# Kernel tuning notes

Measured on AMD Instinct MI355X. Metric: run time of the kernel, lower is better.

## Reference

```python
import jax, jax.numpy as jnp
import numpy as np


def _prelu(x, a):
    return jnp.where(x >= 0, x, a * x)


def _conv1x1(x, w, b, a):
    # x: [N,C,H,W], w: [O,C], b: [O] -> PReLU(conv1x1(x))
    y = jnp.einsum('oc,nchw->nohw', w, x) + b[None, :, None, None]
    return _prelu(y, a)


def setup_inputs() -> dict:
    key = jax.random.key(0)
    ks = jax.random.split(key, 8)
    N, C, H, W = 4, 128, 64, 64
    Cr = C // 2  # reduction=2
    sC = 1.0 / np.sqrt(C)
    x = jax.random.normal(ks[0], (N, C, H, W), dtype=jnp.float32)
    w1 = jax.random.normal(ks[1], (Cr, C), dtype=jnp.float32) * sC
    b1 = jnp.zeros((Cr,), dtype=jnp.float32)
    a1 = jnp.asarray(0.25, dtype=jnp.float32)  # PReLU (single shared slope)
    w2 = jax.random.normal(ks[2], (Cr, C), dtype=jnp.float32) * sC
    b2 = jnp.zeros((Cr,), dtype=jnp.float32)
    a2 = jnp.asarray(0.25, dtype=jnp.float32)
    wa = jax.random.normal(ks[3], (C, C), dtype=jnp.float32) * sC
    ba = jnp.zeros((C,), dtype=jnp.float32)
    aa = jnp.asarray(0.25, dtype=jnp.float32)
    return {"x": x, "w1": w1, "b1": b1, "a1": a1,
            "w2": w2, "b2": b2, "a2": a2,
            "wa": wa, "ba": ba, "aa": aa}


def reference(x, w1, b1, a1, w2, b2, a2, wa, ba, aa):
    N, C, H, W = x.shape
    HW = H * W
    e1 = _conv1x1(x, w1, b1, a1).reshape(N, -1, HW)   # [N,Cr,HW]
    e2 = _conv1x1(x, w2, b2, a2).reshape(N, -1, HW)   # [N,Cr,HW]
    asm = _conv1x1(x, wa, ba, aa).reshape(N, C, HW)   # [N,C,HW]
    # ksize=1: per-channel outer products summed over channels == single contraction
    score = jnp.einsum('nci,ncj->nij', e1, e2)        # [N,HW,HW]
    score = jax.nn.softmax(score, axis=2)
    out = jnp.einsum('nij,ncj->nci', score, asm)      # [N,C,HW]
    return out.reshape(N, C, H, W)
```

## Files before the change

### kernel.cpp

```cpp
#include <hip/hip_runtime.h>
#include <hip/hip_bf16.h>
#include <stdint.h>


typedef float   f32x16 __attribute__((ext_vector_type(16)));
typedef __bf16  bf16x8 __attribute__((ext_vector_type(8)));
typedef __bf16  bf16x2 __attribute__((ext_vector_type(2)));
typedef unsigned int u32x4 __attribute__((ext_vector_type(4)));
typedef unsigned int u32x2 __attribute__((ext_vector_type(2)));

#define L2E 1.4426950408889634f

#define Q_OFF   (0u)
#define KF_OFF  (2u << 20)
#define VF_OFF  (4u << 20)
#define DEN_OFF (8u << 20)
#define WH_OFF  ((8u << 20) + (1u << 19))
#define WL_OFF  (WH_OFF + (1u << 16))
#define OP_OFF  (9u << 20)

__device__ inline unsigned short f2bf(float f) {
  unsigned u = __builtin_bit_cast(unsigned, f);
  return (unsigned short)((u + 0x7FFFu + ((u >> 16) & 1u)) >> 16);
}
__device__ inline float bf2f(unsigned short h) {
  unsigned u = ((unsigned)h) << 16;
  return __builtin_bit_cast(float, u);
}

__global__ void wcast_kernel(const float* __restrict__ w1, const float* __restrict__ w2,
                             const float* __restrict__ wa, char* __restrict__ ws) {
  int idx = blockIdx.x * 256 + threadIdx.x;
  unsigned short* WH = (unsigned short*)(ws + WH_OFF);
  unsigned short* WL = (unsigned short*)(ws + WL_OFF);
#pragma unroll
  for (int r = 0; r < 4; ++r) {
    int i = r * 8192 + idx;
    int oc = i >> 7, c = i & 127;
    float v = oc < 64 ? w1[oc * 128 + c]
            : (oc < 128 ? w2[(oc - 64) * 128 + c] : wa[(oc - 128) * 128 + c]);
    unsigned short h = f2bf(v);
    WH[i] = h;
    WL[i] = f2bf(v - bf2f(h));
  }
}

__global__ __launch_bounds__(256) void conv_kernel(
    const float* __restrict__ x, char* __restrict__ ws,
    const float* __restrict__ b1, const float* __restrict__ a1,
    const float* __restrict__ b2, const float* __restrict__ a2,
    const float* __restrict__ ba, const float* __restrict__ aa) {
  int bid = blockIdx.x;
  int n = bid >> 7, st = bid & 127;
  int sb = st * 32;
  int tid = threadIdx.x;
  int wid = tid >> 6, lane = tid & 63, l31 = lane & 31, hi = lane >> 5;

  __shared__ float xl[128][36];
  __shared__ float tl[2][64][33];
  float* vl = (float*)xl;

  const float* xb = x + (size_t)n * 128 * 4096;
#pragma unroll
  for (int it = 0; it < 4; ++it) {
    int flat4 = tid + 256 * it;
    int c = flat4 >> 3, s4 = flat4 & 7;
    float4 v = *(const float4*)(xb + (size_t)c * 4096 + sb + s4 * 4);
    *(float4*)&xl[c][s4 * 4] = v;
  }
  __syncthreads();

  const char* WH = ws + WH_OFF;
  const char* WL = ws + WL_OFF;
  int oc0 = wid * 64;

  f32x16 acc[2];
  acc[0] = 0.f; acc[1] = 0.f;
#pragma unroll
  for (int c0 = 0; c0 < 8; ++c0) {
    __bf16 eh[8], el[8];
#pragma unroll
    for (int j = 0; j < 8; ++j) {
      float v = xl[c0 * 16 + hi * 8 + j][l31];
      __bf16 h = (__bf16)v;
      eh[j] = h;
      el[j] = (__bf16)(v - (float)h);
    }
    bf16x8 xh = {eh[0], eh[1], eh[2], eh[3], eh[4], eh[5], eh[6], eh[7]};
    bf16x8 xlo = {el[0], el[1], el[2], el[3], el[4], el[5], el[6], el[7]};
#pragma unroll
    for (int mb = 0; mb < 2; ++mb) {
      size_t wo = (size_t)(oc0 + mb * 32 + l31) * 256 + c0 * 32 + hi * 16;
      bf16x8 wh = *(const bf16x8*)(WH + wo);
      bf16x8 wl = *(const bf16x8*)(WL + wo);
      acc[mb] = __builtin_amdgcn_mfma_f32_32x32x16_bf16(wh, xh, acc[mb], 0, 0, 0);
      acc[mb] = __builtin_amdgcn_mfma_f32_32x32x16_bf16(wh, xlo, acc[mb], 0, 0, 0);
      acc[mb] = __builtin_amdgcn_mfma_f32_32x32x16_bf16(wl, xh, acc[mb], 0, 0, 0);
    }
  }
  __syncthreads();

  if (wid < 2) {
    const float* bb = wid ? b2 : b1;
    float slope = wid ? a2[0] : a1[0];
    float scl = wid ? 1.0f : L2E;
#pragma unroll
    for (int mb = 0; mb < 2; ++mb)
#pragma unroll
      for (int reg = 0; reg < 16; ++reg) {
        int row = mb * 32 + (reg & 3) + 8 * (reg >> 2) + 4 * hi;
        float y = acc[mb][reg] + bb[row];
        y = fmaxf(y, 0.f) + slope * fminf(y, 0.f);
        tl[wid][row][l31] = y * scl;
      }
  } else {
    float slope = aa[0];
#pragma unroll
    for (int mb = 0; mb < 2; ++mb)
#pragma unroll
      for (int reg = 0; reg < 16; ++reg) {
        int dv = (wid - 2) * 64 + mb * 32 + (reg & 3) + 8 * (reg >> 2) + 4 * hi;
        float y = acc[mb][reg] + ba[dv];
        y = fmaxf(y, 0.f) + slope * fminf(y, 0.f);
        vl[dv * 33 + l31] = y;
      }
  }
  __syncthreads();

  if (wid == 0) {
    char* Qg = ws + Q_OFF + (size_t)n * (4096 * 128);
#pragma unroll
    for (int it = 0; it < 4; ++it) {
      int sl = (lane >> 3) + it * 8;
      unsigned short u[8];
#pragma unroll
      for (int i = 0; i < 8; ++i) u[i] = f2bf(tl[0][(lane & 7) * 8 + i][sl]);
      u32x4 pv;
      pv.x = ((unsigned)u[1] << 16) | u[0]; pv.y = ((unsigned)u[3] << 16) | u[2];
      pv.z = ((unsigned)u[5] << 16) | u[4]; pv.w = ((unsigned)u[7] << 16) | u[6];
      *(u32x4*)(Qg + (size_t)(sb + sl) * 128 + (lane & 7) * 16) = pv;
    }
  } else if (wid == 1) {
    char* KFb = ws + KF_OFF + (size_t)n * (512 << 10);
    int d0 = (lane & 7) >> 1, hs = lane & 1;
#pragma unroll
    for (int it = 0; it < 4; ++it) {
      int sl = (lane >> 3) + it * 8;
      unsigned short u[8];
#pragma unroll
      for (int i = 0; i < 8; ++i) u[i] = f2bf(tl[1][(lane & 7) * 8 + i][sl]);
      u32x4 pv;
      pv.x = ((unsigned)u[1] << 16) | u[0]; pv.y = ((unsigned)u[3] << 16) | u[2];
      pv.z = ((unsigned)u[5] << 16) | u[4]; pv.w = ((unsigned)u[7] << 16) | u[6];
      *(u32x4*)(KFb + ((size_t)(st * 4 + d0) * 64 + hs * 32 + sl) * 16) = pv;
    }
  }
  {
    char* VFb = ws + VF_OFF + (size_t)n * (1u << 20);
#pragma unroll
    for (int r = 0; r < 2; ++r) {
      int u = tid + r * 256;
      int dv = u >> 2, sc = u & 3;
      unsigned short b[8];
#pragma unroll
      for (int i = 0; i < 8; ++i) b[i] = f2bf(vl[dv * 33 + sc * 8 + i]);
      u32x4 pv;
      pv.x = ((unsigned)b[1] << 16) | b[0]; pv.y = ((unsigned)b[3] << 16) | b[2];
      pv.z = ((unsigned)b[5] << 16) | b[4]; pv.w = ((unsigned)b[7] << 16) | b[6];
      int unit = st * 8 + (dv >> 5) * 2 + (sc >> 1);
      *(u32x4*)(VFb + ((size_t)unit * 64 + (sc & 1) * 32 + (dv & 31)) * 16) = pv;
    }
  }
}

__global__ __launch_bounds__(256, 2) void attn_kernel(char* __restrict__ ws) {
  int bid = blockIdx.x;
  int split = bid & 7;
  int qt = (bid >> 3) & 31;
  int batch = bid >> 8;
  int tid = threadIdx.x;
  int wid = tid >> 6, lane = tid & 63, l31 = lane & 31, hi = lane >> 5;

  const char* Qb  = ws + Q_OFF  + (size_t)batch * (4096 * 128);
  const char* Kt0 = ws + KF_OFF + (size_t)batch * (512 << 10) +
                    (size_t)(split * 16) * 4096;
  const char* Vt0 = ws + VF_OFF + (size_t)batch * (1u << 20) +
                    (size_t)(split * 16) * 8192;

  int q0 = qt * 128 + wid * 32;

  bf16x8 qf[4];
#pragma unroll
  for (int d0 = 0; d0 < 4; ++d0)
    qf[d0] = *(const bf16x8*)(Qb + (size_t)(q0 + l31) * 128 + d0 * 32 + hi * 16);

  f32x16 oacc[4];
#pragma unroll
  for (int i = 0; i < 4; ++i) oacc[i] = 0.f;
  float den0 = 0.f, den1 = 0.f, den2 = 0.f, den3 = 0.f;

  bf16x8 kf[2][4], vf[2][8];
  int lo16 = lane * 16;
#pragma unroll
  for (int u = 0; u < 4; ++u)
    kf[0][u] = *(const bf16x8*)(Kt0 + u * 1024 + lo16);
#pragma unroll
  for (int u = 0; u < 8; ++u)
    vf[0][u] = *(const bf16x8*)(Vt0 + u * 1024 + lo16);

#pragma unroll
  for (int t = 0; t < 16; ++t) {
    const int cur = t & 1, nxt = cur ^ 1;
    if (t + 1 < 16) {
#pragma unroll
      for (int u = 0; u < 4; ++u)
        kf[nxt][u] = *(const bf16x8*)(Kt0 + (t + 1) * 4096 + u * 1024 + lo16);
#pragma unroll
      for (int u = 0; u < 8; ++u)
        vf[nxt][u] = *(const bf16x8*)(Vt0 + (t + 1) * 8192 + u * 1024 + lo16);
    }

    f32x16 sacc;
    sacc = 0.f;
    __builtin_amdgcn_s_setprio(1);
#pragma unroll
    for (int d0 = 0; d0 < 4; ++d0)
      sacc = __builtin_amdgcn_mfma_f32_32x32x16_bf16(kf[cur][d0], qf[d0],
                                                     sacc, 0, 0, 0);
    __builtin_amdgcn_s_setprio(0);

    unsigned pk[8];
#pragma unroll
    for (int m = 0; m < 8; ++m) {
      float e0 = __builtin_amdgcn_exp2f(sacc[2 * m]);
      float e1 = __builtin_amdgcn_exp2f(sacc[2 * m + 1]);
      if ((m & 3) == 0) den0 += e0 + e1;
      else if ((m & 3) == 1) den1 += e0 + e1;
      else if ((m & 3) == 2) den2 += e0 + e1;
      else den3 += e0 + e1;
      bf16x2 bp = { (__bf16)e0, (__bf16)e1 };
      pk[m] = __builtin_bit_cast(unsigned, bp);
    }

#pragma unroll
    for (int kc = 0; kc < 2; ++kc) {
      const int bs = kc * 4;
      u32x2 r0 = __builtin_amdgcn_permlane32_swap(pk[bs + 0], pk[bs + 2],
                                                  false, false);
      u32x2 r1 = __builtin_amdgcn_permlane32_swap(pk[bs + 1], pk[bs + 3],
                                                  false, false);
      u32x4 pu = {r0.x, r1.x, r0.y, r1.y};
      bf16x8 pf = __builtin_bit_cast(bf16x8, pu);
      __builtin_amdgcn_s_setprio(1);
#pragma unroll
      for (int dvb = 0; dvb < 4; ++dvb)
        oacc[dvb] = __builtin_amdgcn_mfma_f32_32x32x16_bf16(
            vf[cur][dvb * 2 + kc], pf, oacc[dvb], 0, 0, 0);
      __builtin_amdgcn_s_setprio(0);
    }
  }

  unsigned short* OPu = (unsigned short*)(ws + OP_OFF) +
                        (size_t)((batch * 32 + qt) * 8 + split) * 16384;
  int qloc = wid * 32 + l31;
#pragma unroll
  for (int dvb = 0; dvb < 4; ++dvb)
#pragma unroll
    for (int reg = 0; reg < 16; ++reg) {
      int dv = dvb * 32 + (reg & 3) + 8 * (reg >> 2) + 4 * hi;
      __builtin_nontemporal_store(f2bf(oacc[dvb][reg]), &OPu[dv * 128 + qloc]);
    }
  float den = (den0 + den1) + (den2 + den3);
  float dtot = den + __shfl_xor(den, 32, 64);
  if (hi == 0) {
    float* DEN = (float*)(ws + DEN_OFF) +
                 (size_t)((batch * 32 + qt) * 8 + split) * 128;
    DEN[qloc] = dtot;
  }
}

__global__ __launch_bounds__(256) void combine_kernel(const char* __restrict__ ws,
                                                      float* __restrict__ out) {
  int idx = blockIdx.x * 256 + threadIdx.x;
  int n = idx >> 19;
  int dv = (idx >> 12) & 127;
  int s = idx & 4095;
  int qt = s >> 7, ql = s & 127;
  const unsigned short* OPu = (const unsigned short*)(ws + OP_OFF);
  const float* DEN = (const float*)(ws + DEN_OFF);
  size_t pb = (size_t)((n * 32 + qt) * 8);
  float num = 0.f, den = 0.f;
#pragma unroll
  for (int h = 0; h < 8; ++h) {
    num += bf2f(__builtin_nontemporal_load(
        &OPu[(pb + h) * 16384 + (size_t)dv * 128 + ql]));
    den += DEN[(pb + h) * 128 + ql];
  }
  __builtin_nontemporal_store(num / den, &out[idx]);
}

extern "C" void kernel_launch(void* const* d_in, const int* in_sizes, int n_in,
                              void* d_out, int out_size, void* d_ws, size_t ws_size,
                              hipStream_t stream) {
  (void)in_sizes; (void)n_in; (void)out_size; (void)ws_size;
  const float* x  = (const float*)d_in[0];
  const float* w1 = (const float*)d_in[1];
  const float* b1 = (const float*)d_in[2];
  const float* a1 = (const float*)d_in[3];
  const float* w2 = (const float*)d_in[4];
  const float* b2 = (const float*)d_in[5];
  const float* a2 = (const float*)d_in[6];
  const float* wa = (const float*)d_in[7];
  const float* ba = (const float*)d_in[8];
  const float* aa = (const float*)d_in[9];
  char* ws = (char*)d_ws;
  float* out = (float*)d_out;

  wcast_kernel<<<dim3(32), dim3(256), 0, stream>>>(w1, w2, wa, ws);
  conv_kernel<<<dim3(512), dim3(256), 0, stream>>>(x, ws, b1, a1, b2, a2, ba, aa);
  attn_kernel<<<dim3(1024), dim3(256), 0, stream>>>(ws);
  combine_kernel<<<dim3(8192), dim3(256), 0, stream>>>(ws, out);
}
```

Measured before the change: 69.92 us.

## Stage K/V through LDS with async loads, software-pipeline attention, vectorize combine

The attention kernel now copies each K/V tile into a triple-buffered shared-memory ring with global_load_lds and computes QK^T for step t while running exp and PV for step t-1. This software pipeline is meant to hide load latency and overlap MFMA with the exponentials. Register-held K/V double buffers are gone and the occupancy hint rises from 2 to 3 blocks, at the cost of per-step block barriers and extra LDS reads. The combine kernel handles 8 outputs per thread with vector loads and stores, the conv epilogue packs pairs to bf16 with native converts, and several nontemporal hints are dropped.

Measured after the change: 66.52 us. 4.9% less time.

```diff
diff --git a/kernel.cpp b/kernel.cpp
--- a/kernel.cpp
+++ b/kernel.cpp
@@ -26,6 +26,16 @@
 __device__ inline float bf2f(unsigned short h) {
   unsigned u = ((unsigned)h) << 16;
   return __builtin_bit_cast(float, u);
+}
+__device__ inline unsigned pack2(float a, float b) {
+  bf16x2 t = { (__bf16)a, (__bf16)b };
+  return __builtin_bit_cast(unsigned, t);
+}
+
+__device__ inline void gld_lds16(const void* g, void* l) {
+  __builtin_amdgcn_global_load_lds(
+      (const __attribute__((address_space(1))) unsigned*)g,
+      (__attribute__((address_space(3))) unsigned*)l, 16, 0, 0);
 }
 
 __global__ void wcast_kernel(const float* __restrict__ w1, const float* __restrict__ w2,
@@ -132,12 +142,11 @@
 #pragma unroll
     for (int it = 0; it < 4; ++it) {
       int sl = (lane >> 3) + it * 8;
-      unsigned short u[8];
-#pragma unroll
-      for (int i = 0; i < 8; ++i) u[i] = f2bf(tl[0][(lane & 7) * 8 + i][sl]);
       u32x4 pv;
-      pv.x = ((unsigned)u[1] << 16) | u[0]; pv.y = ((unsigned)u[3] << 16) | u[2];
-      pv.z = ((unsigned)u[5] << 16) | u[4]; pv.w = ((unsigned)u[7] << 16) | u[6];
+#pragma unroll
+      for (int p = 0; p < 4; ++p)
+        pv[p] = pack2(tl[0][(lane & 7) * 8 + 2 * p][sl],
+                      tl[0][(lane & 7) * 8 + 2 * p + 1][sl]);
       *(u32x4*)(Qg + (size_t)(sb + sl) * 128 + (lane & 7) * 16) = pv;
     }
   } else if (wid == 1) {
@@ -146,12 +155,11 @@
 #pragma unroll
     for (int it = 0; it < 4; ++it) {
       int sl = (lane >> 3) + it * 8;
-      unsigned short u[8];
-#pragma unroll
-      for (int i = 0; i < 8; ++i) u[i] = f2bf(tl[1][(lane & 7) * 8 + i][sl]);
       u32x4 pv;
-      pv.x = ((unsigned)u[1] << 16) | u[0]; pv.y = ((unsigned)u[3] << 16) | u[2];
-      pv.z = ((unsigned)u[5] << 16) | u[4]; pv.w = ((unsigned)u[7] << 16) | u[6];
+#pragma unroll
+      for (int p = 0; p < 4; ++p)
+        pv[p] = pack2(tl[1][(lane & 7) * 8 + 2 * p][sl],
+                      tl[1][(lane & 7) * 8 + 2 * p + 1][sl]);
       *(u32x4*)(KFb + ((size_t)(st * 4 + d0) * 64 + hs * 32 + sl) * 16) = pv;
     }
   }
@@ -161,19 +169,17 @@
     for (int r = 0; r < 2; ++r) {
       int u = tid + r * 256;
       int dv = u >> 2, sc = u & 3;
-      unsigned short b[8];
-#pragma unroll
-      for (int i = 0; i < 8; ++i) b[i] = f2bf(vl[dv * 33 + sc * 8 + i]);
       u32x4 pv;
-      pv.x = ((unsigned)b[1] << 16) | b[0]; pv.y = ((unsigned)b[3] << 16) | b[2];
-      pv.z = ((unsigned)b[5] << 16) | b[4]; pv.w = ((unsigned)b[7] << 16) | b[6];
+#pragma unroll
+      for (int p = 0; p < 4; ++p)
+        pv[p] = pack2(vl[dv * 33 + sc * 8 + 2 * p], vl[dv * 33 + sc * 8 + 2 * p + 1]);
       int unit = st * 8 + (dv >> 5) * 2 + (sc >> 1);
       *(u32x4*)(VFb + ((size_t)unit * 64 + (sc & 1) * 32 + (dv & 31)) * 16) = pv;
     }
   }
 }
 
-__global__ __launch_bounds__(256, 2) void attn_kernel(char* __restrict__ ws) {
+__global__ __launch_bounds__(256, 3) void attn_kernel(char* __restrict__ ws) {
   int bid = blockIdx.x;
   int split = bid & 7;
   int qt = (bid >> 3) & 31;
@@ -187,7 +193,10 @@
   const char* Vt0 = ws + VF_OFF + (size_t)batch * (1u << 20) +
                     (size_t)(split * 16) * 8192;
 
+  __shared__ char sbuf[3][12288];
+
   int q0 = qt * 128 + wid * 32;
+  int lo16 = lane * 16;
 
   bf16x8 qf[4];
 #pragma unroll
@@ -197,51 +206,99 @@
   f32x16 oacc[4];
 #pragma unroll
   for (int i = 0; i < 4; ++i) oacc[i] = 0.f;
-  float den0 = 0.f, den1 = 0.f, den2 = 0.f, den3 = 0.f;
-
-  bf16x8 kf[2][4], vf[2][8];
-  int lo16 = lane * 16;
-#pragma unroll
-  for (int u = 0; u < 4; ++u)
-    kf[0][u] = *(const bf16x8*)(Kt0 + u * 1024 + lo16);
-#pragma unroll
-  for (int u = 0; u < 8; ++u)
-    vf[0][u] = *(const bf16x8*)(Vt0 + u * 1024 + lo16);
-
-#pragma unroll
-  for (int t = 0; t < 16; ++t) {
-    const int cur = t & 1, nxt = cur ^ 1;
-    if (t + 1 < 16) {
-#pragma unroll
-      for (int u = 0; u < 4; ++u)
-        kf[nxt][u] = *(const bf16x8*)(Kt0 + (t + 1) * 4096 + u * 1024 + lo16);
-#pragma unroll
-      for (int u = 0; u < 8; ++u)
-        vf[nxt][u] = *(const bf16x8*)(Vt0 + (t + 1) * 8192 + u * 1024 + lo16);
-    }
-
-    f32x16 sacc;
-    sacc = 0.f;
+  float den0 = 0.f, den1 = 0.f;
+
+  auto stage = [&](int b, int t) {
+#pragma unroll
+    for (int i = 0; i < 3; ++i) {
+      int c = wid * 3 + i;
+      const char* src = (c < 4) ? Kt0 + (size_t)t * 4096 + c * 1024 + lo16
+                                : Vt0 + (size_t)t * 8192 + (c - 4) * 1024 + lo16;
+      gld_lds16(src, &sbuf[b][c * 1024]);
+    }
+  };
+
+  f32x16 sacc[2];
+  unsigned pk[8];
+
+  stage(0, 0);
+  __syncthreads();
+  stage(1, 1);
+  {
+    f32x16 s;
+    s = 0.f;
     __builtin_amdgcn_s_setprio(1);
 #pragma unroll
-    for (int d0 = 0; d0 < 4; ++d0)
-      sacc = __builtin_amdgcn_mfma_f32_32x32x16_bf16(kf[cur][d0], qf[d0],
-                                                     sacc, 0, 0, 0);
+    for (int d0 = 0; d0 < 4; ++d0) {
+      bf16x8 kf = *(const bf16x8*)(&sbuf[0][d0 * 1024 + lo16]);
+      s = __builtin_amdgcn_mfma_f32_32x32x16_bf16(kf, qf[d0], s, 0, 0, 0);
+    }
     __builtin_amdgcn_s_setprio(0);
-
-    unsigned pk[8];
+    sacc[0] = s;
+  }
+  __syncthreads();
+  stage(2, 2);
+
+#pragma unroll
+  for (int t = 1; t < 16; ++t) {
+    {
+      const char* kb = sbuf[t % 3];
+      f32x16 s;
+      s = 0.f;
+      __builtin_amdgcn_s_setprio(1);
+#pragma unroll
+      for (int d0 = 0; d0 < 4; ++d0) {
+        bf16x8 kf = *(const bf16x8*)(kb + d0 * 1024 + lo16);
+        s = __builtin_amdgcn_mfma_f32_32x32x16_bf16(kf, qf[d0], s, 0, 0, 0);
+      }
+      __builtin_amdgcn_s_setprio(0);
+      sacc[t & 1] = s;
+    }
+    {
+      f32x16 sp = sacc[(t - 1) & 1];
+#pragma unroll
+      for (int m = 0; m < 8; ++m) {
+        float e0 = __builtin_amdgcn_exp2f(sp[2 * m]);
+        float e1 = __builtin_amdgcn_exp2f(sp[2 * m + 1]);
+        if (m & 1) den1 += e0 + e1; else den0 += e0 + e1;
+        pk[m] = pack2(e0, e1);
+      }
+    }
+    {
+      const char* vb = sbuf[(t - 1) % 3] + 4096;
+#pragma unroll
+      for (int kc = 0; kc < 2; ++kc) {
+        const int bs = kc * 4;
+        u32x2 r0 = __builtin_amdgcn_permlane32_swap(pk[bs + 0], pk[bs + 2],
+                                                    false, false);
+        u32x2 r1 = __builtin_amdgcn_permlane32_swap(pk[bs + 1], pk[bs + 3],
+                                                    false, false);
+        u32x4 pu = {r0.x, r1.x, r0.y, r1.y};
+        bf16x8 pf = __builtin_bit_cast(bf16x8, pu);
+        __builtin_amdgcn_s_setprio(1);
+#pragma unroll
+        for (int dvb = 0; dvb < 4; ++dvb) {
+          bf16x8 vf = *(const bf16x8*)(vb + (dvb * 2 + kc) * 1024 + lo16);
+          oacc[dvb] = __builtin_amdgcn_mfma_f32_32x32x16_bf16(vf, pf,
+                                                              oacc[dvb], 0, 0, 0);
+        }
+        __builtin_amdgcn_s_setprio(0);
+      }
+    }
+    __syncthreads();
+    if (t + 2 < 16) stage((t + 2) % 3, t + 2);
+  }
+
+  {
+    f32x16 sp = sacc[15 & 1];
 #pragma unroll
     for (int m = 0; m < 8; ++m) {
-      float e0 = __builtin_amdgcn_exp2f(sacc[2 * m]);
-      float e1 = __builtin_amdgcn_exp2f(sacc[2 * m + 1]);
-      if ((m & 3) == 0) den0 += e0 + e1;
-      else if ((m & 3) == 1) den1 += e0 + e1;
-      else if ((m & 3) == 2) den2 += e0 + e1;
-      else den3 += e0 + e1;
-      bf16x2 bp = { (__bf16)e0, (__bf16)e1 };
-      pk[m] = __builtin_bit_cast(unsigned, bp);
-    }
-
+      float e0 = __builtin_amdgcn_exp2f(sp[2 * m]);
+      float e1 = __builtin_amdgcn_exp2f(sp[2 * m + 1]);
+      if (m & 1) den1 += e0 + e1; else den0 += e0 + e1;
+      pk[m] = pack2(e0, e1);
+    }
+    const char* vb = sbuf[15 % 3] + 4096;
 #pragma unroll
     for (int kc = 0; kc < 2; ++kc) {
       const int bs = kc * 4;
@@ -251,12 +308,12 @@
                                                   false, false);
       u32x4 pu = {r0.x, r1.x, r0.y, r1.y};
       bf16x8 pf = __builtin_bit_cast(bf16x8, pu);
-      __builtin_amdgcn_s_setprio(1);
-#pragma unroll
-      for (int dvb = 0; dvb < 4; ++dvb)
-        oacc[dvb] = __builtin_amdgcn_mfma_f32_32x32x16_bf16(
-            vf[cur][dvb * 2 + kc], pf, oacc[dvb], 0, 0, 0);
-      __builtin_amdgcn_s_setprio(0);
+#pragma unroll
+      for (int dvb = 0; dvb < 4; ++dvb) {
+        bf16x8 vf = *(const bf16x8*)(vb + (dvb * 2 + kc) * 1024 + lo16);
+        oacc[dvb] = __builtin_amdgcn_mfma_f32_32x32x16_bf16(vf, pf,
+                                                            oacc[dvb], 0, 0, 0);
+      }
     }
   }
 
@@ -268,9 +325,9 @@
 #pragma unroll
     for (int reg = 0; reg < 16; ++reg) {
       int dv = dvb * 32 + (reg & 3) + 8 * (reg >> 2) + 4 * hi;
-      __builtin_nontemporal_store(f2bf(oacc[dvb][reg]), &OPu[dv * 128 + qloc]);
-    }
-  float den = (den0 + den1) + (den2 + den3);
+      OPu[dv * 128 + qloc] = f2bf(oacc[dvb][reg]);
+    }
+  float den = den0 + den1;
   float dtot = den + __shfl_xor(den, 32, 64);
   if (hi == 0) {
     float* DEN = (float*)(ws + DEN_OFF) +
@@ -281,22 +338,32 @@
 
 __global__ __launch_bounds__(256) void combine_kernel(const char* __restrict__ ws,
                                                       float* __restrict__ out) {
-  int idx = blockIdx.x * 256 + threadIdx.x;
-  int n = idx >> 19;
-  int dv = (idx >> 12) & 127;
-  int s = idx & 4095;
-  int qt = s >> 7, ql = s & 127;
+  int idx8 = (blockIdx.x * 256 + threadIdx.x) * 8;
+  int n = idx8 >> 19;
+  int dv = (idx8 >> 12) & 127;
+  int s0 = idx8 & 4095;
+  int qt = s0 >> 7, ql = s0 & 127;
   const unsigned short* OPu = (const unsigned short*)(ws + OP_OFF);
   const float* DEN = (const float*)(ws + DEN_OFF);
   size_t pb = (size_t)((n * 32 + qt) * 8);
-  float num = 0.f, den = 0.f;
+  float num[8], den[8];
+#pragma unroll
+  for (int j = 0; j < 8; ++j) { num[j] = 0.f; den[j] = 0.f; }
 #pragma unroll
   for (int h = 0; h < 8; ++h) {
-    num += bf2f(__builtin_nontemporal_load(
-        &OPu[(pb + h) * 16384 + (size_t)dv * 128 + ql]));
-    den += DEN[(pb + h) * 128 + ql];
-  }
-  __builtin_nontemporal_store(num / den, &out[idx]);
+    bf16x8 v = *(const bf16x8*)(OPu + (pb + h) * 16384 + (size_t)dv * 128 + ql);
+    const float* dp = DEN + (pb + h) * 128 + ql;
+    float4 d0 = *(const float4*)dp;
+    float4 d1 = *(const float4*)(dp + 4);
+#pragma unroll
+    for (int j = 0; j < 8; ++j) num[j] += (float)v[j];
+    den[0] += d0.x; den[1] += d0.y; den[2] += d0.z; den[3] += d0.w;
+    den[4] += d1.x; den[5] += d1.y; den[6] += d1.z; den[7] += d1.w;
+  }
+  float4 o0 = {num[0] / den[0], num[1] / den[1], num[2] / den[2], num[3] / den[3]};
+  float4 o1 = {num[4] / den[4], num[5] / den[5], num[6] / den[6], num[7] / den[7]};
+  *(float4*)&out[idx8] = o0;
+  *(float4*)&out[idx8 + 4] = o1;
 }
 
 extern "C" void kernel_launch(void* const* d_in, const int* in_sizes, int n_in,
@@ -319,5 +386,5 @@
   wcast_kernel<<<dim3(32), dim3(256), 0, stream>>>(w1, w2, wa, ws);
   conv_kernel<<<dim3(512), dim3(256), 0, stream>>>(x, ws, b1, a1, b2, a2, ba, aa);
   attn_kernel<<<dim3(1024), dim3(256), 0, stream>>>(ws);
-  combine_kernel<<<dim3(8192), dim3(256), 0, stream>>>(ws, out);
-}
+  combine_kernel<<<dim3(1024), dim3(256), 0, stream>>>(ws, out);
+}
```
